# Kernel optimization log

Hardware: AMD Instinct MI355X
Metric: run time of the kernel (lower is better)

## Reference

```python
import jax, jax.numpy as jnp
import numpy as np

N = 100000   # node_size
R = 1000     # rel_size
T = 600000   # triple_size (edges)
D = 128      # node_dim
DEPTH = 2


def seg_softmax(logits, seg, num_segments):
    # softmax over irregular segments (rows of a sparse [N,N] matrix)
    m = jax.lax.stop_gradient(jax.ops.segment_max(logits, seg, num_segments=num_segments))
    e = jnp.exp(logits - m[seg])
    s = jax.ops.segment_sum(e, seg, num_segments=num_segments)
    return e / s[seg]


def setup_inputs() -> dict:
    key = jax.random.key(0)
    ks = jax.random.split(key, 10)
    xav = float(np.sqrt(6.0 / (D + 1)))
    features = jax.random.normal(ks[0], (N, D), dtype=jnp.float32)
    rel_emb = jax.random.normal(ks[1], (R, D), dtype=jnp.float32)
    # adj: (2, T) COO edges; rows sorted to mimic coalesced sparse tensor
    adj_row = jnp.sort(jax.random.randint(ks[2], (T,), 0, N))
    adj_col = jax.random.randint(ks[3], (T,), 0, N)
    adj = jnp.stack([adj_row, adj_col]).astype(jnp.int64)
    # r_index: (2, T) indices of sparse [T, R] matrix, one relation per triple
    r_index = jnp.stack([jnp.arange(T), jax.random.randint(ks[4], (T,), 0, R)]).astype(jnp.int64)
    r_val = jax.random.uniform(ks[5], (T,), dtype=jnp.float32)
    hn_row = jnp.sort(jax.random.randint(ks[6], (T,), 0, N))
    hn_col = jax.random.randint(ks[7], (T,), 0, N)
    high_nei = jnp.stack([hn_row, hn_col]).astype(jnp.int64)
    attn_kernels = jax.random.uniform(ks[8], (DEPTH, D, 1), jnp.float32, -xav, xav)
    high_atts = jax.random.uniform(ks[9], (DEPTH, D, 1), jnp.float32, -xav, xav)
    return {"features": features, "rel_emb": rel_emb, "r_val": r_val,
            "attn_kernels": attn_kernels, "high_atts": high_atts,
            "adj": adj, "r_index": r_index, "high_nei": high_nei}


def reference(features, rel_emb, r_val, attn_kernels, high_atts, adj, r_index, high_nei):
    row, col = adj[0], adj[1]
    hrow, hcol = high_nei[0], high_nei[1]
    outputs = []
    feats = jnp.tanh(features)
    outputs.append(feats)
    for l in range(DEPTH):
        # sparse [T,R] @ rel_emb -> per-triple relation embedding [T,D]
        tri_rel = jax.ops.segment_sum(r_val[:, None] * rel_emb[r_index[1]],
                                      r_index[0], num_segments=T)
        tri_rel = tri_rel / jnp.maximum(
            jnp.linalg.norm(tri_rel, axis=1, keepdims=True), 1e-12)
        neighs = feats[col]                                   # [T,D] gather
        # Householder reflection of neighbor features across tri_rel
        neighs = neighs - 2.0 * jnp.sum(neighs * tri_rel, axis=1, keepdims=True) * tri_rel
        att = (tri_rel @ attn_kernels[l])[:, 0]               # [T]
        att = seg_softmax(att, row, N)                        # sparse row softmax
        feats = jnp.tanh(jax.ops.segment_sum(neighs * att[:, None], row, num_segments=N))
        outputs.append(feats)
    for l in range(DEPTH):
        neighs = feats[hcol]                                  # [T,D]
        att = seg_softmax((neighs @ high_atts[l])[:, 0], hrow, N)
        feats = jnp.tanh(jax.ops.segment_sum(neighs * att[:, None], hrow, num_segments=N))
        outputs.append(feats)
    return jnp.concatenate(outputs, axis=-1)                  # [N, D*(2*DEPTH+1)]
```

## Files before the change

kernel.cpp:

```cpp
#include <hip/hip_runtime.h>
#include <math.h>

#define N_NODES 100000
#define R_REL   1000
#define T_TRI   600000
#define D_DIM   128
#define OUT_STRIDE 640

typedef unsigned int  u32;
typedef unsigned short u16;

template<int CTRL>
__device__ __forceinline__ float dpp_add(float x) {
    int xi = __float_as_int(x);
    int r = __builtin_amdgcn_update_dpp(xi, xi, CTRL, 0xf, 0xf, false);
    return x + __int_as_float(r);
}
__device__ __forceinline__ float row16_sum(float v) {
    v = dpp_add<0x121>(v);
    v = dpp_add<0x122>(v);
    v = dpp_add<0x124>(v);
    v = dpp_add<0x128>(v);
    return v;
}
__device__ __forceinline__ float wave_sum(float v) {
    #pragma unroll
    for (int off = 32; off > 0; off >>= 1) v += __shfl_xor(v, off);
    return v;
}
__device__ __forceinline__ float half32_sum(float v) {
    v = row16_sum(v);
    v += __shfl_xor(v, 16);
    return v;
}
__device__ __forceinline__ float fast_tanh(float x) {
    float e = __expf(2.f * x);
    return 1.f - __fdividef(2.f, e + 1.f);
}
__device__ __forceinline__ float4 tanh4(float4 v) {
    float4 o; o.x = fast_tanh(v.x); o.y = fast_tanh(v.y);
    o.z = fast_tanh(v.z); o.w = fast_tanh(v.w);
    return o;
}
__device__ __forceinline__ float dot4(float4 a, float4 b) {
    return a.x*b.x + a.y*b.y + a.z*b.z + a.w*b.w;
}
__device__ __forceinline__ u32 bfr(float x) {
    u32 u = __float_as_uint(x);
    return (u + 0x7fffu + ((u >> 16) & 1u)) >> 16;
}
__device__ __forceinline__ uint2 pack_bf4(float4 v) {
    uint2 p;
    p.x = bfr(v.x) | (bfr(v.y) << 16);
    p.y = bfr(v.z) | (bfr(v.w) << 16);
    return p;
}
__device__ __forceinline__ void unpack_bf8(uint4 v, float f[8]) {
    f[0] = __uint_as_float(v.x << 16); f[1] = __uint_as_float(v.x & 0xffff0000u);
    f[2] = __uint_as_float(v.y << 16); f[3] = __uint_as_float(v.y & 0xffff0000u);
    f[4] = __uint_as_float(v.z << 16); f[5] = __uint_as_float(v.z & 0xffff0000u);
    f[6] = __uint_as_float(v.w << 16); f[7] = __uint_as_float(v.w & 0xffff0000u);
}

__global__ void k_prep(const float* __restrict__ feat, const float* __restrict__ rel,
                       const float* __restrict__ attk,
                       float* __restrict__ out, u16* __restrict__ bf0,
                       u16* __restrict__ relu_bf, float* __restrict__ wtab,
                       const int* __restrict__ adj_rows, const int* __restrict__ hn_rows,
                       int* __restrict__ rpa, int* __restrict__ rph) {
    int tid = threadIdx.x;
    int gt = blockIdx.x * blockDim.x + tid;
    int gstride = gridDim.x * blockDim.x;

    for (int i = gt; i < N_NODES * D_DIM / 4; i += gstride) {
        int n = i >> 5, d4 = i & 31;
        float4 v = ((const float4*)feat)[i];
        float4 t = tanh4(v);
        ((float4*)(out + (size_t)n * OUT_STRIDE))[d4] = t;
        ((uint2*)(bf0 + (size_t)n * D_DIM))[d4] = pack_bf4(t);
    }
    int gw = gt >> 6, lane = tid & 63;
    int nwaves = gstride >> 6;
    for (int r = gw; r < R_REL; r += nwaves) {
        float2 a  = ((const float2*)rel)[r * 64 + lane];
        float2 k0 = ((const float2*)attk)[lane];
        float2 k1 = ((const float2*)(attk + D_DIM))[lane];
        float nrm2 = wave_sum(a.x * a.x + a.y * a.y);
        float d0 = wave_sum(a.x * k0.x + a.y * k0.y);
        float d1 = wave_sum(a.x * k1.x + a.y * k1.y);
        float inv = __frsqrt_rn(nrm2);
        ((u32*)relu_bf)[r * 64 + lane] = bfr(a.x * inv) | (bfr(a.y * inv) << 16);
        if (lane == 0) {
            wtab[r]         = __expf(d0 * inv);
            wtab[R_REL + r] = __expf(d1 * inv);
        }
    }
    for (int i = gt; i < 2 * (N_NODES + 1); i += gstride) {
        const int* rows; int* p; int n;
        if (i <= N_NODES) { rows = adj_rows; p = rpa; n = i; }
        else { rows = hn_rows; p = rph; n = i - (N_NODES + 1); }
        int lo = 0, hi = T_TRI;
        while (lo < hi) { int m = (lo + hi) >> 1; if (rows[m] < n) lo = m + 1; else hi = m; }
        p[n] = lo;
    }
}

__global__ __launch_bounds__(256) void k_nr_layer(
    float* __restrict__ outbuf, int out_off,
    const u16* __restrict__ in_bf,
    u16* __restrict__ out_bf,
    const int* __restrict__ row_ptr,
    const int* __restrict__ col,
    const int* __restrict__ ridx1,
    const float* __restrict__ r_val,
    const u16* __restrict__ relu_bf,
    const float* __restrict__ wtab,
    const float* __restrict__ ha,
    float* __restrict__ eproj_out) {
    __shared__ float s_w[4][64];
    int wslot = threadIdx.x >> 6;
    int lane  = threadIdx.x & 63;
    int wid2  = (blockIdx.x * blockDim.x + threadIdx.x) >> 6;
    int row   = wid2 * 2 + (lane >> 5);
    if (row >= N_NODES) return;
    int ll  = lane & 31;
    int sgl = (lane >> 4) & 1;
    int sl  = lane & 15;
    int beg = row_ptr[row], end = row_ptr[row + 1];
    int deg = end - beg;
    float* orow = outbuf + (size_t)row * OUT_STRIDE + out_off;

    if (deg == 0) {
        float4 z = {0.f,0.f,0.f,0.f};
        ((float4*)orow)[ll] = z;
        if (out_bf != nullptr && ll < 16) {
            uint4 zz = {0u,0u,0u,0u};
            ((uint4*)(out_bf + (size_t)row * D_DIM))[ll] = zz;
        }
        if (ha != nullptr && ll == 0) eproj_out[row] = 1.f;
        return;
    }

    int  t0 = beg + ll;
    bool va = t0 < end;
    int  ta = va ? t0 : beg;
    int  rt_a = ridx1[ta];
    float rv_a = r_val[ta];
    bool  z_a  = (rv_a == 0.f);
    float w_a  = va ? (z_a ? 1.f : wtab[rt_a]) : 0.f;

    int  tb0 = beg + sgl, tb1 = beg + 2 + sgl;
    bool v0 = tb0 < end, v1 = tb1 < end;
    int  tc0 = v0 ? tb0 : beg, tc1 = v1 ? tb1 : beg;
    int  cc0 = col[tc0],   cc1 = col[tc1];
    int  rr0 = ridx1[tc0], rr1 = ridx1[tc1];
    uint4 F0 = ((const uint4*)(in_bf   + (size_t)cc0 * D_DIM))[sl];
    uint4 U0 = ((const uint4*)(relu_bf + (size_t)rr0 * D_DIM))[sl];
    uint4 F1 = ((const uint4*)(in_bf   + (size_t)cc1 * D_DIM))[sl];
    uint4 U1 = ((const uint4*)(relu_bf + (size_t)rr1 * D_DIM))[sl];

    float lsum = w_a;
    for (int t = t0 + 32; t < end; t += 32) {
        int rt = ridx1[t]; float rv = r_val[t];
        lsum += (rv == 0.f) ? 1.f : wtab[rt];
    }
    float inv_s = 1.f / half32_sum(lsum);
    float sw = w_a * inv_s;
    s_w[wslot][lane] = z_a ? -sw : sw;
    int hb = lane & 32;

    float sv = s_w[wslot][hb + sgl];
    float w0 = fabsf(sv);
    float nf[8], uf[8];
    unpack_bf8(F0, nf); unpack_bf8(U0, uf);
    float pd = 0.f;
    #pragma unroll
    for (int j = 0; j < 8; ++j) pd += nf[j] * uf[j];
    pd = row16_sum(pd);
    float b0 = (sv < 0.f) ? 0.f : 2.f * w0 * pd;
    float acc[8];
    #pragma unroll
    for (int j = 0; j < 8; ++j) acc[j] = w0 * nf[j] - b0 * uf[j];

    int niter = (deg + 1) >> 1;
    int cur_tc = tc1, cur_rr = rr1; bool cur_v = v1;
    for (int it = 1; it < niter; ++it) {
        int tb = beg + 2 * (it + 1) + sgl;
        bool nv = tb < end;
        int  ntc = nv ? tb : beg;
        int  ncc = col[ntc];
        int  nrr = ridx1[ntc];
        uint4 NF = ((const uint4*)(in_bf   + (size_t)ncc * D_DIM))[sl];
        uint4 NU = ((const uint4*)(relu_bf + (size_t)nrr * D_DIM))[sl];

        int idx = 2 * it + sgl;
        float sv2;
        if (idx < 32) sv2 = s_w[wslot][hb + idx];
        else {
            float rv = r_val[cur_tc];
            bool z = (rv == 0.f);
            float wv = cur_v ? (z ? 1.f : wtab[cur_rr]) * inv_s : 0.f;
            sv2 = z ? -wv : wv;
        }
        float w = fabsf(sv2);
        float gf[8], qf[8];
        unpack_bf8(F1, gf); unpack_bf8(U1, qf);
        float pdt = 0.f;
        #pragma unroll
        for (int j = 0; j < 8; ++j) pdt += gf[j] * qf[j];
        pdt = row16_sum(pdt);
        float bt = (sv2 < 0.f) ? 0.f : 2.f * w * pdt;
        #pragma unroll
        for (int j = 0; j < 8; ++j) acc[j] += w * gf[j] - bt * qf[j];

        F1 = NF; U1 = NU;
        cur_tc = ntc; cur_rr = nrr; cur_v = nv;
    }

    #pragma unroll
    for (int j = 0; j < 8; ++j) acc[j] += __shfl_xor(acc[j], 16);

    float4 q = (sgl == 0) ? make_float4(acc[0], acc[1], acc[2], acc[3])
                          : make_float4(acc[4], acc[5], acc[6], acc[7]);
    float4 tq = tanh4(q);
    ((float4*)orow)[2 * sl + sgl] = tq;
    if (out_bf != nullptr)
        ((uint2*)(out_bf + (size_t)row * D_DIM))[2 * sl + sgl] = pack_bf4(tq);
    if (ha != nullptr) {
        const float4* ha4 = (const float4*)ha;
        float pdp = dot4(tq, ha4[2 * sl + sgl]);
        pdp = row16_sum(pdp);
        pdp += __shfl_xor(pdp, 16);
        if (ll == 0) eproj_out[row] = __expf(pdp);
    }
}

__global__ __launch_bounds__(256) void k_high_layer(
    float* __restrict__ outbuf, int out_off,
    const u16* __restrict__ in_bf,
    u16* __restrict__ out_bf,
    const int* __restrict__ row_ptr,
    const int* __restrict__ hcol,
    const float* __restrict__ eproj,
    const float* __restrict__ ha,
    float* __restrict__ eproj_out) {
    __shared__ float s_w[4][64];
    int wslot = threadIdx.x >> 6;
    int lane  = threadIdx.x & 63;
    int wid2  = (blockIdx.x * blockDim.x + threadIdx.x) >> 6;
    int row   = wid2 * 2 + (lane >> 5);
    if (row >= N_NODES) return;
    int ll  = lane & 31;
    int sgl = (lane >> 4) & 1;
    int sl  = lane & 15;
    int beg = row_ptr[row], end = row_ptr[row + 1];
    int deg = end - beg;
    float* orow = outbuf + (size_t)row * OUT_STRIDE + out_off;

    if (deg == 0) {
        float4 z = {0.f,0.f,0.f,0.f};
        ((float4*)orow)[ll] = z;
        if (out_bf != nullptr && ll < 16) {
            uint4 zz = {0u,0u,0u,0u};
            ((uint4*)(out_bf + (size_t)row * D_DIM))[ll] = zz;
        }
        if (ha != nullptr && ll == 0) eproj_out[row] = 1.f;
        return;
    }

    int  t0 = beg + ll;
    bool va = t0 < end;
    int  ta = va ? t0 : beg;
    int  c_a = hcol[ta];
    float e_a = eproj[c_a];
    e_a = va ? e_a : 0.f;

    int  tb0 = beg + sgl, tb1 = beg + 2 + sgl;
    bool v0 = tb0 < end, v1 = tb1 < end;
    int  tc0 = v0 ? tb0 : beg, tc1 = v1 ? tb1 : beg;
    int  cc0 = hcol[tc0], cc1 = hcol[tc1];
    uint4 F0 = ((const uint4*)(in_bf + (size_t)cc0 * D_DIM))[sl];
    uint4 F1 = ((const uint4*)(in_bf + (size_t)cc1 * D_DIM))[sl];

    float lsum = e_a;
    for (int t = t0 + 32; t < end; t += 32)
        lsum += eproj[hcol[t]];
    float inv_s = 1.f / half32_sum(lsum);
    s_w[wslot][lane] = e_a * inv_s;
    int hb = lane & 32;

    float w0 = s_w[wslot][hb + sgl];
    float nf[8];
    unpack_bf8(F0, nf);
    float acc[8];
    #pragma unroll
    for (int j = 0; j < 8; ++j) acc[j] = w0 * nf[j];

    int niter = (deg + 1) >> 1;
    int cur_cc = cc1; bool cur_v = v1;
    for (int it = 1; it < niter; ++it) {
        int tb = beg + 2 * (it + 1) + sgl;
        bool nv = tb < end;
        int  ntc = nv ? tb : beg;
        int  ncc = hcol[ntc];
        uint4 NF = ((const uint4*)(in_bf + (size_t)ncc * D_DIM))[sl];

        int idx = 2 * it + sgl;
        float w;
        if (idx < 32) w = s_w[wslot][hb + idx];
        else          w = cur_v ? eproj[cur_cc] * inv_s : 0.f;
        float gf[8];
        unpack_bf8(F1, gf);
        #pragma unroll
        for (int j = 0; j < 8; ++j) acc[j] += w * gf[j];

        F1 = NF; cur_cc = ncc; cur_v = nv;
    }

    #pragma unroll
    for (int j = 0; j < 8; ++j) acc[j] += __shfl_xor(acc[j], 16);

    float4 q = (sgl == 0) ? make_float4(acc[0], acc[1], acc[2], acc[3])
                          : make_float4(acc[4], acc[5], acc[6], acc[7]);
    float4 tq = tanh4(q);
    ((float4*)orow)[2 * sl + sgl] = tq;
    if (out_bf != nullptr)
        ((uint2*)(out_bf + (size_t)row * D_DIM))[2 * sl + sgl] = pack_bf4(tq);
    if (ha != nullptr) {
        const float4* ha4 = (const float4*)ha;
        float pdp = dot4(tq, ha4[2 * sl + sgl]);
        pdp = row16_sum(pdp);
        pdp += __shfl_xor(pdp, 16);
        if (ll == 0) eproj_out[row] = __expf(pdp);
    }
}

extern "C" void kernel_launch(void* const* d_in, const int* in_sizes, int n_in,
                              void* d_out, int out_size, void* d_ws, size_t ws_size,
                              hipStream_t stream) {
    const float* features  = (const float*)d_in[0];
    const float* rel_emb   = (const float*)d_in[1];
    const float* r_val     = (const float*)d_in[2];
    const float* attk      = (const float*)d_in[3];
    const float* high_atts = (const float*)d_in[4];
    const int*   adj       = (const int*)d_in[5];
    const int*   r_index   = (const int*)d_in[6];
    const int*   high_nei  = (const int*)d_in[7];
    float* out = (float*)d_out;

    char* ws = (char*)d_ws;
    auto take = [&](size_t bytes) -> char* {
        char* p = ws;
        ws += (bytes + 255) & ~(size_t)255;
        return p;
    };
    int*   row_ptr_adj  = (int*)take((N_NODES + 1) * sizeof(int));
    int*   row_ptr_high = (int*)take((N_NODES + 1) * sizeof(int));
    float* wtab         = (float*)take(2 * R_REL * sizeof(float));
    float* eproj0       = (float*)take(N_NODES * sizeof(float));
    float* eproj1       = (float*)take(N_NODES * sizeof(float));
    u16*   relu_bf      = (u16*)take((size_t)R_REL * D_DIM * sizeof(u16));
    u16*   fbf0         = (u16*)take((size_t)N_NODES * D_DIM * sizeof(u16));
    u16*   fbf1         = (u16*)take((size_t)N_NODES * D_DIM * sizeof(u16));
    u16*   fbf2         = (u16*)take((size_t)N_NODES * D_DIM * sizeof(u16));
    u16*   fbf3         = (u16*)take((size_t)N_NODES * D_DIM * sizeof(u16));

    k_prep<<<4096, 256, 0, stream>>>(features, rel_emb, attk, out, fbf0,
                                     relu_bf, wtab, adj, high_nei,
                                     row_ptr_adj, row_ptr_high);

    int pair_blocks = ((N_NODES + 1) / 2 + 3) / 4;

    k_nr_layer<<<pair_blocks, 256, 0, stream>>>(
        out, 1 * D_DIM, fbf0, fbf1,
        row_ptr_adj, adj + T_TRI, r_index + T_TRI, r_val,
        relu_bf, wtab + 0 * R_REL, nullptr, nullptr);
    k_nr_layer<<<pair_blocks, 256, 0, stream>>>(
        out, 2 * D_DIM, fbf1, fbf2,
        row_ptr_adj, adj + T_TRI, r_index + T_TRI, r_val,
        relu_bf, wtab + 1 * R_REL, high_atts + 0 * D_DIM, eproj0);
    k_high_layer<<<pair_blocks, 256, 0, stream>>>(
        out, 3 * D_DIM, fbf2, fbf3,
        row_ptr_high, high_nei + T_TRI, eproj0, high_atts + 1 * D_DIM, eproj1);
    k_high_layer<<<pair_blocks, 256, 0, stream>>>(
        out, 4 * D_DIM, fbf3, nullptr,
        row_ptr_high, high_nei + T_TRI, eproj1, nullptr, nullptr);
}
```

Baseline: 209.0 us.

## Pack edge col/relation/zero-flag into int2 and drop manual prefetch pipelining

Adds a pass in the prep kernel that packs each edge's column, relation index and a zero-r_val flag into one int2 array. The layer kernels then read that single array instead of three separate ones. Both layer kernels drop their hand-rolled double-buffered prefetch of neighbor rows for a plain loop, and gain a launch_bounds occupancy hint of 8 blocks. The aim is fewer index loads and lower register pressure so more waves can hide gather latency. The cost is an extra 600k-edge pack pass and losing explicit load/compute overlap.

Result: slower. 214.2 us (+2.4%).

```diff
diff --git a/kernel.cpp b/kernel.cpp
--- a/kernel.cpp
+++ b/kernel.cpp
@@ -63,11 +63,13 @@
 }
 
 __global__ void k_prep(const float* __restrict__ feat, const float* __restrict__ rel,
-                       const float* __restrict__ attk,
+                       const float* __restrict__ attk, const float* __restrict__ r_val,
                        float* __restrict__ out, u16* __restrict__ bf0,
                        u16* __restrict__ relu_bf, float* __restrict__ wtab,
-                       const int* __restrict__ adj_rows, const int* __restrict__ hn_rows,
-                       int* __restrict__ rpa, int* __restrict__ rph) {
+                       const int* __restrict__ adj, const int* __restrict__ r_index,
+                       const int* __restrict__ hn_rows,
+                       int* __restrict__ rpa, int* __restrict__ rph,
+                       int2* __restrict__ epack) {
     int tid = threadIdx.x;
     int gt = blockIdx.x * blockDim.x + tid;
     int gstride = gridDim.x * blockDim.x;
@@ -97,22 +99,26 @@
     }
     for (int i = gt; i < 2 * (N_NODES + 1); i += gstride) {
         const int* rows; int* p; int n;
-        if (i <= N_NODES) { rows = adj_rows; p = rpa; n = i; }
+        if (i <= N_NODES) { rows = adj; p = rpa; n = i; }
         else { rows = hn_rows; p = rph; n = i - (N_NODES + 1); }
         int lo = 0, hi = T_TRI;
         while (lo < hi) { int m = (lo + hi) >> 1; if (rows[m] < n) lo = m + 1; else hi = m; }
         p[n] = lo;
     }
-}
-
-__global__ __launch_bounds__(256) void k_nr_layer(
+    for (int t = gt; t < T_TRI; t += gstride) {
+        int c  = adj[T_TRI + t];
+        int rt = r_index[T_TRI + t];
+        if (r_val[t] == 0.f) rt |= 0x80000000;
+        epack[t] = make_int2(c, rt);
+    }
+}
+
+__global__ __launch_bounds__(256, 8) void k_nr_layer(
     float* __restrict__ outbuf, int out_off,
     const u16* __restrict__ in_bf,
     u16* __restrict__ out_bf,
     const int* __restrict__ row_ptr,
-    const int* __restrict__ col,
-    const int* __restrict__ ridx1,
-    const float* __restrict__ r_val,
+    const int2* __restrict__ epack,
     const u16* __restrict__ relu_bf,
     const float* __restrict__ wtab,
     const float* __restrict__ ha,
@@ -143,78 +149,48 @@
 
     int  t0 = beg + ll;
     bool va = t0 < end;
-    int  ta = va ? t0 : beg;
-    int  rt_a = ridx1[ta];
-    float rv_a = r_val[ta];
-    bool  z_a  = (rv_a == 0.f);
-    float w_a  = va ? (z_a ? 1.f : wtab[rt_a]) : 0.f;
-
-    int  tb0 = beg + sgl, tb1 = beg + 2 + sgl;
-    bool v0 = tb0 < end, v1 = tb1 < end;
-    int  tc0 = v0 ? tb0 : beg, tc1 = v1 ? tb1 : beg;
-    int  cc0 = col[tc0],   cc1 = col[tc1];
-    int  rr0 = ridx1[tc0], rr1 = ridx1[tc1];
-    uint4 F0 = ((const uint4*)(in_bf   + (size_t)cc0 * D_DIM))[sl];
-    uint4 U0 = ((const uint4*)(relu_bf + (size_t)rr0 * D_DIM))[sl];
-    uint4 F1 = ((const uint4*)(in_bf   + (size_t)cc1 * D_DIM))[sl];
-    uint4 U1 = ((const uint4*)(relu_bf + (size_t)rr1 * D_DIM))[sl];
-
+    int2 ea = epack[va ? t0 : beg];
+    int  rt_a = ea.y & 0x7fffffff;
+    bool z_a  = ea.y < 0;
+    float w_a = va ? (z_a ? 1.f : wtab[rt_a]) : 0.f;
     float lsum = w_a;
     for (int t = t0 + 32; t < end; t += 32) {
-        int rt = ridx1[t]; float rv = r_val[t];
-        lsum += (rv == 0.f) ? 1.f : wtab[rt];
+        int2 e = epack[t];
+        lsum += (e.y < 0) ? 1.f : wtab[e.y & 0x7fffffff];
     }
     float inv_s = 1.f / half32_sum(lsum);
     float sw = w_a * inv_s;
     s_w[wslot][lane] = z_a ? -sw : sw;
     int hb = lane & 32;
 
-    float sv = s_w[wslot][hb + sgl];
-    float w0 = fabsf(sv);
-    float nf[8], uf[8];
-    unpack_bf8(F0, nf); unpack_bf8(U0, uf);
-    float pd = 0.f;
-    #pragma unroll
-    for (int j = 0; j < 8; ++j) pd += nf[j] * uf[j];
-    pd = row16_sum(pd);
-    float b0 = (sv < 0.f) ? 0.f : 2.f * w0 * pd;
-    float acc[8];
-    #pragma unroll
-    for (int j = 0; j < 8; ++j) acc[j] = w0 * nf[j] - b0 * uf[j];
-
+    float acc[8] = {0.f,0.f,0.f,0.f,0.f,0.f,0.f,0.f};
     int niter = (deg + 1) >> 1;
-    int cur_tc = tc1, cur_rr = rr1; bool cur_v = v1;
-    for (int it = 1; it < niter; ++it) {
-        int tb = beg + 2 * (it + 1) + sgl;
-        bool nv = tb < end;
-        int  ntc = nv ? tb : beg;
-        int  ncc = col[ntc];
-        int  nrr = ridx1[ntc];
-        uint4 NF = ((const uint4*)(in_bf   + (size_t)ncc * D_DIM))[sl];
-        uint4 NU = ((const uint4*)(relu_bf + (size_t)nrr * D_DIM))[sl];
-
+    for (int it = 0; it < niter; ++it) {
         int idx = 2 * it + sgl;
-        float sv2;
-        if (idx < 32) sv2 = s_w[wslot][hb + idx];
+        int t = beg + idx;
+        bool valid = t < end;
+        int2 e = epack[valid ? t : beg];
+        int c  = e.x;
+        int rt = e.y & 0x7fffffff;
+        float sv;
+        if (idx < 32) sv = s_w[wslot][hb + idx];
         else {
-            float rv = r_val[cur_tc];
-            bool z = (rv == 0.f);
-            float wv = cur_v ? (z ? 1.f : wtab[cur_rr]) * inv_s : 0.f;
-            sv2 = z ? -wv : wv;
+            bool z = e.y < 0;
+            float wv = valid ? (z ? 1.f : wtab[rt]) * inv_s : 0.f;
+            sv = z ? -wv : wv;
         }
-        float w = fabsf(sv2);
-        float gf[8], qf[8];
-        unpack_bf8(F1, gf); unpack_bf8(U1, qf);
-        float pdt = 0.f;
+        float w = fabsf(sv);
+        uint4 F = ((const uint4*)(in_bf   + (size_t)c  * D_DIM))[sl];
+        uint4 U = ((const uint4*)(relu_bf + (size_t)rt * D_DIM))[sl];
+        float nf[8], uf[8];
+        unpack_bf8(F, nf); unpack_bf8(U, uf);
+        float pd = 0.f;
         #pragma unroll
-        for (int j = 0; j < 8; ++j) pdt += gf[j] * qf[j];
-        pdt = row16_sum(pdt);
-        float bt = (sv2 < 0.f) ? 0.f : 2.f * w * pdt;
+        for (int j = 0; j < 8; ++j) pd += nf[j] * uf[j];
+        pd = row16_sum(pd);
+        float bt = (sv < 0.f) ? 0.f : 2.f * w * pd;
         #pragma unroll
-        for (int j = 0; j < 8; ++j) acc[j] += w * gf[j] - bt * qf[j];
-
-        F1 = NF; U1 = NU;
-        cur_tc = ntc; cur_rr = nrr; cur_v = nv;
+        for (int j = 0; j < 8; ++j) acc[j] += w * nf[j] - bt * uf[j];
     }
 
     #pragma unroll
@@ -235,7 +211,7 @@
     }
 }
 
-__global__ __launch_bounds__(256) void k_high_layer(
+__global__ __launch_bounds__(256, 8) void k_high_layer(
     float* __restrict__ outbuf, int out_off,
     const u16* __restrict__ in_bf,
     u16* __restrict__ out_bf,
@@ -270,18 +246,7 @@
 
     int  t0 = beg + ll;
     bool va = t0 < end;
-    int  ta = va ? t0 : beg;
-    int  c_a = hcol[ta];
-    float e_a = eproj[c_a];
-    e_a = va ? e_a : 0.f;
-
-    int  tb0 = beg + sgl, tb1 = beg + 2 + sgl;
-    bool v0 = tb0 < end, v1 = tb1 < end;
-    int  tc0 = v0 ? tb0 : beg, tc1 = v1 ? tb1 : beg;
-    int  cc0 = hcol[tc0], cc1 = hcol[tc1];
-    uint4 F0 = ((const uint4*)(in_bf + (size_t)cc0 * D_DIM))[sl];
-    uint4 F1 = ((const uint4*)(in_bf + (size_t)cc1 * D_DIM))[sl];
-
+    float e_a = va ? eproj[hcol[va ? t0 : beg]] : 0.f;
     float lsum = e_a;
     for (int t = t0 + 32; t < end; t += 32)
         lsum += eproj[hcol[t]];
@@ -289,32 +254,21 @@
     s_w[wslot][lane] = e_a * inv_s;
     int hb = lane & 32;
 
-    float w0 = s_w[wslot][hb + sgl];
-    float nf[8];
-    unpack_bf8(F0, nf);
-    float acc[8];
-    #pragma unroll
-    for (int j = 0; j < 8; ++j) acc[j] = w0 * nf[j];
-
+    float acc[8] = {0.f,0.f,0.f,0.f,0.f,0.f,0.f,0.f};
     int niter = (deg + 1) >> 1;
-    int cur_cc = cc1; bool cur_v = v1;
-    for (int it = 1; it < niter; ++it) {
-        int tb = beg + 2 * (it + 1) + sgl;
-        bool nv = tb < end;
-        int  ntc = nv ? tb : beg;
-        int  ncc = hcol[ntc];
-        uint4 NF = ((const uint4*)(in_bf + (size_t)ncc * D_DIM))[sl];
-
+    for (int it = 0; it < niter; ++it) {
         int idx = 2 * it + sgl;
+        int t = beg + idx;
+        bool valid = t < end;
+        int c = hcol[valid ? t : beg];
         float w;
         if (idx < 32) w = s_w[wslot][hb + idx];
-        else          w = cur_v ? eproj[cur_cc] * inv_s : 0.f;
-        float gf[8];
-        unpack_bf8(F1, gf);
+        else          w = valid ? eproj[c] * inv_s : 0.f;
+        uint4 F = ((const uint4*)(in_bf + (size_t)c * D_DIM))[sl];
+        float nf[8];
+        unpack_bf8(F, nf);
         #pragma unroll
-        for (int j = 0; j < 8; ++j) acc[j] += w * gf[j];
-
-        F1 = NF; cur_cc = ncc; cur_v = nv;
+        for (int j = 0; j < 8; ++j) acc[j] += w * nf[j];
     }
 
     #pragma unroll
@@ -359,26 +313,26 @@
     float* wtab         = (float*)take(2 * R_REL * sizeof(float));
     float* eproj0       = (float*)take(N_NODES * sizeof(float));
     float* eproj1       = (float*)take(N_NODES * sizeof(float));
+    int2*  epack        = (int2*)take((size_t)T_TRI * sizeof(int2));
     u16*   relu_bf      = (u16*)take((size_t)R_REL * D_DIM * sizeof(u16));
     u16*   fbf0         = (u16*)take((size_t)N_NODES * D_DIM * sizeof(u16));
     u16*   fbf1         = (u16*)take((size_t)N_NODES * D_DIM * sizeof(u16));
     u16*   fbf2         = (u16*)take((size_t)N_NODES * D_DIM * sizeof(u16));
     u16*   fbf3         = (u16*)take((size_t)N_NODES * D_DIM * sizeof(u16));
 
-    k_prep<<<4096, 256, 0, stream>>>(features, rel_emb, attk, out, fbf0,
-                                     relu_bf, wtab, adj, high_nei,
-                                     row_ptr_adj, row_ptr_high);
+    k_prep<<<4096, 256, 0, stream>>>(features, rel_emb, attk, r_val, out, fbf0,
+                                     relu_bf, wtab, adj, r_index, high_nei,
+                                     row_ptr_adj, row_ptr_high, epack);
 
     int pair_blocks = ((N_NODES + 1) / 2 + 3) / 4;
 
     k_nr_layer<<<pair_blocks, 256, 0, stream>>>(
         out, 1 * D_DIM, fbf0, fbf1,
-        row_ptr_adj, adj + T_TRI, r_index + T_TRI, r_val,
-        relu_bf, wtab + 0 * R_REL, nullptr, nullptr);
+        row_ptr_adj, epack, relu_bf, wtab + 0 * R_REL, nullptr, nullptr);
     k_nr_layer<<<pair_blocks, 256, 0, stream>>>(
         out, 2 * D_DIM, fbf1, fbf2,
-        row_ptr_adj, adj + T_TRI, r_index + T_TRI, r_val,
-        relu_bf, wtab + 1 * R_REL, high_atts + 0 * D_DIM, eproj0);
+        row_ptr_adj, epack, relu_bf, wtab + 1 * R_REL,
+        high_atts + 0 * D_DIM, eproj0);
     k_high_layer<<<pair_blocks, 256, 0, stream>>>(
         out, 3 * D_DIM, fbf2, fbf3,
         row_ptr_high, high_nei + T_TRI, eproj0, high_atts + 1 * D_DIM, eproj1);
```
